# Performance work log

Measured on AMD Instinct MI355X. Metric: run time of the kernel, lower is better.

The kernel has to match this reference:

```python
import jax, jax.numpy as jnp
import numpy as np

BS, N, D, H = 4, 128, 768, 8
HD = D // H
FFN = 3072
E = BS * N * N
NORM_FACTOR = 100.0
NORM_CONST = 1.0
EPS_LN = 1e-5


def _ln(v, s, b):
    m = jnp.mean(v, -1, keepdims=True)
    var = jnp.mean(jnp.square(v - m), -1, keepdims=True)
    return (v - m) * jax.lax.rsqrt(var + EPS_LN) * s + b


def _glu(v, w, b):
    a, g = jnp.split(v @ w.T + b, 2, axis=-1)
    return a * jnp.square(jax.nn.relu(g))  # GLU with ReLU^2 gate activation


def setup_inputs() -> dict:
    key = jax.random.key(0)
    ks = jax.random.split(key, 24)
    rn = lambda i, shape, s=1.0: jax.random.normal(ks[i], shape, jnp.float32) * s
    # fully-connected per-graph edge_index with block structure
    base = jnp.arange(BS, dtype=jnp.int32) * N
    ii = jnp.repeat(jnp.arange(N, dtype=jnp.int32), N)
    jj = jnp.tile(jnp.arange(N, dtype=jnp.int32), N)
    row = (base[:, None] + ii[None, :]).reshape(-1)
    col = (base[:, None] + jj[None, :]).reshape(-1)
    edge_index = jnp.stack([row, col], 0)  # [2, E]
    return {
        'h': rn(0, (BS * N, D)),
        'x': rn(1, (BS * N, 3)),
        'edge_attr': rn(2, (E, 1)),
        'node_mask': jnp.ones((BS * N, 1), jnp.float32),
        'edge_mask': jnp.ones((E, 1), jnp.float32),
        'linker_mask': jnp.ones((BS * N, 1), jnp.float32),
        'in_proj_w': rn(3, (3 * D, D), 0.02), 'in_proj_b': jnp.zeros((3 * D,)),
        'out_proj_w': rn(4, (D, D), 0.02), 'out_proj_b': jnp.zeros((D,)),
        'ln1_s': jnp.ones((D,)), 'ln1_b': jnp.zeros((D,)),
        'ln2_s': jnp.ones((D,)), 'ln2_b': jnp.zeros((D,)),
        'fc1_w': rn(5, (2 * FFN, D), 0.02), 'fc1_b': jnp.zeros((2 * FFN,)),
        'fc2_w': rn(6, (2 * D, FFN), 0.02), 'fc2_b': jnp.zeros((2 * D,)),
        'efc1_w': rn(7, (H, 2), 0.5), 'efc1_b': jnp.zeros((H,)),
        'efc2_w': rn(8, (H, 2), 0.5), 'efc2_b': jnp.zeros((H,)),
        'cm1_w': rn(9, (D, 2 * D + 2), 0.02), 'cm1_b': jnp.zeros((D,)),
        'cm2_w': rn(10, (D, D), 0.02), 'cm2_b': jnp.zeros((D,)),
        'cm3_w': rn(11, (1, D), 0.001),
        'edge_index': edge_index,
    }


def _forward(h, x, edge_attr, node_mask, edge_mask, linker_mask,
             in_proj_w, in_proj_b, out_proj_w, out_proj_b,
             ln1_s, ln1_b, ln2_s, ln2_b, fc1_w, fc1_b, fc2_w, fc2_b,
             efc1_w, efc1_b, efc2_w, efc2_b,
             cm1_w, cm1_b, cm2_w, cm2_b, cm3_w, edge_index):
    row, col = edge_index[0], edge_index[1]
    # coord2diff
    diff = x[row] - x[col]                                   # [E,3]
    radial = jnp.sum(jnp.square(diff), 1, keepdims=True)     # [E,1]
    coord_diff = diff / (jnp.sqrt(radial + 1e-8) + NORM_CONST)
    ea = jnp.concatenate([radial, edge_attr], 1)             # [E,2]

    def edge_to_heads(w, b):
        y = (ea @ w.T + b) * edge_mask                       # [E,H]
        return jnp.transpose(y.reshape(BS, N, N, H), (0, 3, 1, 2))  # [BS,H,N,N]

    attn_bias = edge_to_heads(efc1_w, efc1_b)
    gw = edge_to_heads(efc2_w, efc2_b)

    # Graphormer3DEncoderLayer (eval mode: dropout = identity)
    hb = h.reshape(BS, N, D)
    hn = _ln(hb, ln1_s, ln1_b)
    q, k, v = jnp.split(hn @ in_proj_w.T + in_proj_b, 3, axis=-1)
    q = q.reshape(BS, N, H, HD) * (HD ** -0.5)
    k = k.reshape(BS, N, H, HD)
    v = v.reshape(BS, N, H, HD)
    scores = jnp.einsum('bihd,bjhd->bhij', q, k) + attn_bias
    probs = jnp.tanh(gw) * jax.nn.softmax(scores, axis=-1)   # tanh-gated softmax
    att = jnp.einsum('bhij,bjhd->bihd', probs, v).reshape(BS, N, D)
    h1 = hb + (att @ out_proj_w.T + out_proj_b)
    ff = _ln(h1, ln2_s, ln2_b)
    ff = jax.nn.gelu(_glu(ff, fc1_w, fc1_b), approximate=False)
    ff = _glu(ff, fc2_w, fc2_b)
    h_out = (h1 + ff).reshape(BS * N, D) * node_mask

    # EquivariantUpdate (tanh=False branch)
    ei = jnp.concatenate([h_out[row], h_out[col], ea], 1)    # [E, 2D+2]
    t = jax.nn.silu(ei @ cm1_w.T + cm1_b)
    t = jax.nn.silu(t @ cm2_w.T + cm2_b)
    s = t @ cm3_w.T                                          # [E,1]
    trans = coord_diff * s * edge_mask
    agg = jax.ops.segment_sum(trans, row, num_segments=BS * N) / NORM_FACTOR
    x_out = (x + agg * linker_mask) * node_mask
    return h_out, x_out


def reference(h, x, edge_attr, node_mask, edge_mask, linker_mask,
              in_proj_w, in_proj_b, out_proj_w, out_proj_b,
              ln1_s, ln1_b, ln2_s, ln2_b, fc1_w, fc1_b, fc2_w, fc2_b,
              efc1_w, efc1_b, efc2_w, efc2_b,
              cm1_w, cm1_b, cm2_w, cm2_b, cm3_w, edge_index):
    return _forward(h, x, edge_attr, node_mask, edge_mask, linker_mask,
                    in_proj_w, in_proj_b, out_proj_w, out_proj_b,
                    ln1_s, ln1_b, ln2_s, ln2_b, fc1_w, fc1_b, fc2_w, fc2_b,
                    efc1_w, efc1_b, efc2_w, efc2_b,
                    cm1_w, cm1_b, cm2_w, cm2_b, cm3_w, edge_index)
```

## Files before the change

kernel.cpp:

```cpp
#include <hip/hip_runtime.h>
#include <cstdint>
#include <cstddef>

#define BSZ   4
#define NN    128
#define DD    768
#define HH    8
#define HD    96
#define FFN   3072
#define NNODE (BSZ*NN)
#define NE    (NNODE*NN)

typedef unsigned short u16;
typedef __bf16 bf16x8 __attribute__((ext_vector_type(8)));
typedef float  f32x4  __attribute__((ext_vector_type(4)));
typedef unsigned short u16x8 __attribute__((ext_vector_type(8)));
typedef unsigned short u16x4 __attribute__((ext_vector_type(4)));
typedef unsigned short u16x2 __attribute__((ext_vector_type(2)));

__device__ __forceinline__ float bf2f(u16 a){
    unsigned u = ((unsigned)a) << 16; float f; __builtin_memcpy(&f, &u, 4); return f;
}
__device__ __forceinline__ u16 f2bf(float f){
    unsigned u; __builtin_memcpy(&u, &f, 4);
// ... 200 lines not shown

template<int MODE>
__global__ __launch_bounds__(256) void gemm_glu2(const u16* __restrict__ A, int lda,
                                                 const u16* __restrict__ B, int ldb,
                                                 const float* __restrict__ bias, int half_off, int K,
                                                 const float* __restrict__ h1f,
                                                 const float* __restrict__ nodemask,
                                                 u16* __restrict__ Cb, int ldc,
                                                 float* __restrict__ Cf){
    __shared__ u16 As[2][64 * 64];
    __shared__ u16 Ba[2][64 * 64];
    __shared__ u16 Bg[2][64 * 64];
    GEMM_PRO(A + (size_t)m0 * lda, B + (size_t)n0 * ldb)
    const u16* Gbase = B + (size_t)(half_off + n0) * ldb;
    f32x4 accA[2][2], accG[2][2];
    #pragma unroll
    for (int i = 0; i < 2; i++)
        #pragma unroll
        for (int j = 0; j < 2; j++){ f32x4 z = {0.f,0.f,0.f,0.f}; accA[i][j] = z; accG[i][j] = z; }

    stage64(As[0], Abase, lda, 0, tid);
    stage64(Ba[0], Bbase, ldb, 0, tid);
    stage64(Bg[0], Gbase, ldb, 0, tid);
    __syncthreads();
    const int NS = K / 64;
    #pragma unroll 1
    for (int s = 0; s < NS; s++){
        const int cur = s & 1;
        if (s + 1 < NS){
            stage64(As[cur ^ 1], Abase, lda, (s + 1) * 64, tid);
            stage64(Ba[cur ^ 1], Bbase, ldb, (s + 1) * 64, tid);
            stage64(Bg[cur ^ 1], Gbase, ldb, (s + 1) * 64, tid);
        }
        const char* ab = (const char*)&As[cur][0];
        const char* bab = (const char*)&Ba[cur][0];
        const char* bgb = (const char*)&Bg[cur][0];
        #pragma unroll
        for (int k0 = 0; k0 < 64; k0 += 32){
            const int kbx = ((k0 + quad * 8) * 2) ^ swz;
            bf16x8 a0  = frag((const u16*)(ab + (wy * 32 + l15) * 128 + kbx));
            bf16x8 a1  = frag((const u16*)(ab + (wy * 32 + 16 + l15) * 128 + kbx));
            bf16x8 ba0 = frag((const u16*)(bab + (wx * 32 + l15) * 128 + kbx));
            bf16x8 ba1 = frag((const u16*)(bab + (wx * 32 + 16 + l15) * 128 + kbx));
            bf16x8 bg0 = frag((const u16*)(bgb + (wx * 32 + l15) * 128 + kbx));
            bf16x8 bg1 = frag((const u16*)(bgb + (wx * 32 + 16 + l15) * 128 + kbx));
            accA[0][0] = mfma16(a0, ba0, accA[0][0]);
            accA[0][1] = mfma16(a0, ba1, accA[0][1]);
            accA[1][0] = mfma16(a1, ba0, accA[1][0]);
            accA[1][1] = mfma16(a1, ba1, accA[1][1]);
            accG[0][0] = mfma16(a0, bg0, accG[0][0]);
            accG[0][1] = mfma16(a0, bg1, accG[0][1]);
            accG[1][0] = mfma16(a1, bg0, accG[1][0]);
            accG[1][1] = mfma16(a1, bg1, accG[1][1]);
        }
        __syncthreads();
    }
    #pragma unroll
    for (int j = 0; j < 2; j++){
        int n = n0 + wx * 32 + j * 16 + l15;
        float bva = bias[n];
        float bvg = bias[half_off + n];
        #pragma unroll
        for (int i = 0; i < 2; i++){
            #pragma unroll
            for (int r = 0; r < 4; r++){
                int m = m0 + wy * 32 + i * 16 + quad * 4 + r;
                float a = accA[i][j][r] + bva;
                float g = accG[i][j][r] + bvg;
                float rg = fmaxf(g, 0.f);
                float t = a * rg * rg;
                if (MODE == 0){
                    float v = 0.5f * t * (1.f + erff(t * 0.70710678118654752f));
                    Cb[(size_t)m * ldc + n] = f2bf(v);
                } else {
                    float v = (t + h1f[(size_t)m * DD + n]) * nodemask[m];
                    Cf[(size_t)m * DD + n] = v;
                    Cb[(size_t)m * DD + n] = f2bf(v);
                }
            }
        }
    }
}

__global__ __launch_bounds__(256) void gemm_bt(const u16* __restrict__ A, int lda,
                                               const float* __restrict__ B, int ldb,
                                               const float* __restrict__ bias,
                                               u16* __restrict__ C, int ldc, int K){
    __shared__ u16 As[64 * 72];
    __shared__ u16 Bs[64 * 72];
    const int tid = threadIdx.x;
    const int m0 = blockIdx.y * 64, n0 = blockIdx.x * 64;
    const int w = tid >> 6, lane = tid & 63, quad = lane >> 4, l15 = lane & 15;
    const int wy = w >> 1, wx = w & 1;
    f32x4 acc[2][2];
    #pragma unroll
    for (int i = 0; i < 2; i++)
        #pragma unroll
        for (int j = 0; j < 2; j++){ f32x4 z = {0.f,0.f,0.f,0.f}; acc[i][j] = z; }

    for (int kk = 0; kk < K; kk += 64){
        stageA(As, A, m0, lda, kk, tid);
        stageBf32(Bs, B, n0, ldb, kk, tid);
        __syncthreads();
        #pragma unroll
        for (int k0 = 0; k0 < 64; k0 += 32){
            int kb = k0 + quad * 8;
            bf16x8 a0 = frag(&As[(wy * 32 + l15) * 72 + kb]);
            bf16x8 a1 = frag(&As[(wy * 32 + 16 + l15) * 72 + kb]);
            bf16x8 b0 = frag(&Bs[(wx * 32 + l15) * 72 + kb]);
            bf16x8 b1 = frag(&Bs[(wx * 32 + 16 + l15) * 72 + kb]);
            acc[0][0] = mfma16(a0, b0, acc[0][0]);
            acc[0][1] = mfma16(a0, b1, acc[0][1]);
            acc[1][0] = mfma16(a1, b0, acc[1][0]);
            acc[1][1] = mfma16(a1, b1, acc[1][1]);
        }
        __syncthreads();
    }
    #pragma unroll
    for (int j = 0; j < 2; j++){
        int n = n0 + wx * 32 + j * 16 + l15;
        float bv = bias[n];
        #pragma unroll
        for (int i = 0; i < 2; i++){
            #pragma unroll
            for (int r = 0; r < 4; r++){
                int m = m0 + wy * 32 + i * 16 + quad * 4 + r;
                C[(size_t)m * ldc + n] = f2bf(acc[i][j][r] + bv);
            }
        }
    }
}

__global__ __launch_bounds__(256) void gemm_proj(const u16* __restrict__ A,
                                                 const float* __restrict__ B,
                                                 const float* __restrict__ bias,
                                                 const float* __restrict__ h,
                                                 float* __restrict__ h1f){
    __shared__ u16 As[64 * 72];
    __shared__ u16 Bs[64 * 72];
    const int tid = threadIdx.x;
    const int m0 = blockIdx.y * 64, n0 = blockIdx.x * 64;
    const int w = tid >> 6, lane = tid & 63, quad = lane >> 4, l15 = lane & 15;
    const int wy = w >> 1, wx = w & 1;
    f32x4 acc[2][2];
    #pragma unroll
    for (int i = 0; i < 2; i++)
        #pragma unroll
        for (int j = 0; j < 2; j++){ f32x4 z = {0.f,0.f,0.f,0.f}; acc[i][j] = z; }

    for (int kk = 0; kk < DD; kk += 64){
        stageA(As, A, m0, DD, kk, tid);
        stageBf32(Bs, B, n0, DD, kk, tid);
        __syncthreads();
        #pragma unroll
        for (int k0 = 0; k0 < 64; k0 += 32){
            int kb = k0 + quad * 8;
            bf16x8 a0 = frag(&As[(wy * 32 + l15) * 72 + kb]);
            bf16x8 a1 = frag(&As[(wy * 32 + 16 + l15) * 72 + kb]);
            bf16x8 b0 = frag(&Bs[(wx * 32 + l15) * 72 + kb]);
            bf16x8 b1 = frag(&Bs[(wx * 32 + 16 + l15) * 72 + kb]);
            acc[0][0] = mfma16(a0, b0, acc[0][0]);
            acc[0][1] = mfma16(a0, b1, acc[0][1]);
            acc[1][0] = mfma16(a1, b0, acc[1][0]);
            acc[1][1] = mfma16(a1, b1, acc[1][1]);
        }
        __syncthreads();
// ... 74 lines not shown
                float rg = fmaxf(g, 0.f);
                float t = a * rg * rg;
                if (MODE == 0){
                    float v = 0.5f * t * (1.f + erff(t * 0.70710678118654752f));
                    Cb[(size_t)m * ldc + n] = f2bf(v);
                } else {
                    float v = (t + h1f[(size_t)m * DD + n]) * nodemask[m];
                    Cf[(size_t)m * DD + n] = v;
                    Cb[(size_t)m * DD + n] = f2bf(v);
                }
            }
        }
    }
}

__global__ __launch_bounds__(256) void gemm_pq(const u16* __restrict__ A,
                                               const float* __restrict__ W,
                                               const float* __restrict__ bias,
                                               u16* __restrict__ C){
    __shared__ u16 As[64 * 72];
    __shared__ u16 Bp[64 * 72];
    __shared__ u16 Bq[64 * 72];
    const int tid = threadIdx.x;
    const int m0 = blockIdx.y * 64, n0 = blockIdx.x * 64;
    const int w = tid >> 6, lane = tid & 63, quad = lane >> 4, l15 = lane & 15;
    const int wy = w >> 1, wx = w & 1;
    f32x4 accP[2][2], accQ[2][2];
    #pragma unroll
    for (int i = 0; i < 2; i++)
        #pragma unroll
        for (int j = 0; j < 2; j++){ f32x4 z = {0.f,0.f,0.f,0.f}; accP[i][j] = z; accQ[i][j] = z; }

    for (int kk = 0; kk < DD; kk += 64){
        stageA(As, A, m0, DD, kk, tid);
        #pragma unroll
        for (int p = 0; p < 8; p++){
            int idx = p * 256 + tid;
            int row = idx >> 5, c2 = idx & 31;
            size_t base = (size_t)(n0 + row) * 1538 + kk + c2 * 2;
            float2 vp = *(const float2*)(W + base);
            float2 vq = *(const float2*)(W + base + 768);
            u16x2 op; op[0] = f2bf(vp.x); op[1] = f2bf(vp.y);
            u16x2 oq; oq[0] = f2bf(vq.x); oq[1] = f2bf(vq.y);
            *(u16x2*)&Bp[row * 72 + c2 * 2] = op;
            *(u16x2*)&Bq[row * 72 + c2 * 2] = oq;
        }
        __syncthreads();
        #pragma unroll
        for (int k0 = 0; k0 < 64; k0 += 32){
            int kb = k0 + quad * 8;
            bf16x8 a0  = frag(&As[(wy * 32 + l15) * 72 + kb]);
            bf16x8 a1  = frag(&As[(wy * 32 + 16 + l15) * 72 + kb]);
            bf16x8 bp0 = frag(&Bp[(wx * 32 + l15) * 72 + kb]);
            bf16x8 bp1 = frag(&Bp[(wx * 32 + 16 + l15) * 72 + kb]);
            bf16x8 bq0 = frag(&Bq[(wx * 32 + l15) * 72 + kb]);
            bf16x8 bq1 = frag(&Bq[(wx * 32 + 16 + l15) * 72 + kb]);
            accP[0][0] = mfma16(a0, bp0, accP[0][0]);
            accP[0][1] = mfma16(a0, bp1, accP[0][1]);
            accP[1][0] = mfma16(a1, bp0, accP[1][0]);
            accP[1][1] = mfma16(a1, bp1, accP[1][1]);
            accQ[0][0] = mfma16(a0, bq0, accQ[0][0]);
            accQ[0][1] = mfma16(a0, bq1, accQ[0][1]);
            accQ[1][0] = mfma16(a1, bq0, accQ[1][0]);
            accQ[1][1] = mfma16(a1, bq1, accQ[1][1]);
        }
        __syncthreads();
    }
    #pragma unroll
    for (int j = 0; j < 2; j++){
        int n = n0 + wx * 32 + j * 16 + l15;
        float bv = bias[n];
        #pragma unroll
        for (int i = 0; i < 2; i++){
            #pragma unroll
            for (int r = 0; r < 4; r++){
                int m = m0 + wy * 32 + i * 16 + quad * 4 + r;
                C[(size_t)m * 1536 + n]       = f2bf(accP[i][j][r] + bv);
                C[(size_t)m * 1536 + 768 + n] = f2bf(accQ[i][j][r]);
            }
        }
    }
}

__global__ __launch_bounds__(128) void attn_k(const u16* __restrict__ qkv,
                                              const float* __restrict__ x,
                                              const float* __restrict__ eattr,
                                              const float* __restrict__ emask,
                                              const float* __restrict__ e1w, const float* __restrict__ e1b,
                                              const float* __restrict__ e2w, const float* __restrict__ e2b,
                                              u16* __restrict__ att){
    __shared__ u16 Ks[NN * 98];
    __shared__ u16 Vs[NN * 98];
    __shared__ float xs[NN * 3];
    __shared__ float qs[HD];
    __shared__ float ps[NN];
    __shared__ float red[2];
    const int tid = threadIdx.x;
    const int h = blockIdx.y, b = blockIdx.z;
    const int i0 = blockIdx.x * 16;

    for (int idx = tid; idx < NN * HD; idx += 128){
        int j = idx / HD, d = idx - j * HD;
        const u16* base = qkv + (size_t)(b * NN + j) * 2304 + h * HD + d;
        Ks[j * 98 + d] = base[DD];
        Vs[j * 98 + d] = base[1536];
    }
    if (tid < NN){
        xs[tid * 3]     = x[(b * NN + tid) * 3];
        xs[tid * 3 + 1] = x[(b * NN + tid) * 3 + 1];
        xs[tid * 3 + 2] = x[(b * NN + tid) * 3 + 2];
    }
    __syncthreads();
    const float w1r = e1w[h * 2], w1a = e1w[h * 2 + 1], b1 = e1b[h];
    const float w2r = e2w[h * 2], w2a = e2w[h * 2 + 1], b2v = e2b[h];
    const int wv = tid >> 6;

    for (int ig = 0; ig < 16; ig++){
        const int i = i0 + ig, ni = b * NN + i;
        if (tid < HD) qs[tid] = bf2f(qkv[(size_t)ni * 2304 + h * HD + tid]) * 0.10206207261596577f;
        __syncthreads();
        const int j = tid;
        float s = 0.f;
        #pragma unroll 8
        for (int d = 0; d < HD; d++) s += qs[d] * bf2f(Ks[j * 98 + d]);
        float d0 = xs[i * 3]     - xs[j * 3];
        float d1 = xs[i * 3 + 1] - xs[j * 3 + 1];
        float d2 = xs[i * 3 + 2] - xs[j * 3 + 2];
        float radial = d0*d0 + d1*d1 + d2*d2;
        int e = ni * NN + j;
        float at = eattr[e], em = emask[e];
        s += (w1r * radial + w1a * at + b1) * em;
        float gw = (w2r * radial + w2a * at + b2v) * em;
        float m1 = wred_max(s);
        if ((tid & 63) == 0) red[wv] = m1;
        __syncthreads();
        float M = fmaxf(red[0], red[1]);
        __syncthreads();
        float ev = __expf(s - M);
        float s1 = wred_sum(ev);
        if ((tid & 63) == 0) red[wv] = s1;
        __syncthreads();
        float S = red[0] + red[1];
        ps[j] = tanhf(gw) * ev / S;
        __syncthreads();
        if (tid < HD){
            float a = 0.f;
            #pragma unroll 8
            for (int jj = 0; jj < NN; jj++) a += ps[jj] * bf2f(Vs[jj * 98 + tid]);
            att[(size_t)ni * DD + h * HD + tid] = f2bf(a);
        }
        __syncthreads();
    }
}

__global__ void prep_k(const float* __restrict__ cm1w, float* __restrict__ c01){
    int idx = blockIdx.x * 256 + threadIdx.x;
    if (idx < 768){
        c01[idx]       = cm1w[(size_t)idx * 1538 + 1536];
        c01[768 + idx] = cm1w[(size_t)idx * 1538 + 1537];
    }
}

__global__ void w2bf_k(const float* __restrict__ W, u16* __restrict__ O, int n){
    int i4 = (blockIdx.x * 256 + threadIdx.x) * 4;
    if (i4 < n){
        float4 v = *(const float4*)(W + i4);
        u16x4 o; o[0] = f2bf(v.x); o[1] = f2bf(v.y); o[2] = f2bf(v.z); o[3] = f2bf(v.w);
        *(u16x4*)&O[i4] = o;
    }
}

__global__ __launch_bounds__(256) void t1_k(const u16* __restrict__ PQ,
                                            const float* __restrict__ c01,
                                            const float* __restrict__ x,
                                            const float* __restrict__ eattr,
                                            u16* __restrict__ T1g){
    int cid = blockIdx.x * 256 + threadIdx.x;
    int e = cid / 96;
    int kc = cid - e * 96;
    int k = kc * 8;
    int r = e >> 7;
    int j = e & 127;
    int b = r >> 7;
    int nc = b * NN + j;
    float d0 = x[r * 3]     - x[nc * 3];
    float d1 = x[r * 3 + 1] - x[nc * 3 + 1];
    float d2 = x[r * 3 + 2] - x[nc * 3 + 2];
    float rad = d0 * d0 + d1 * d1 + d2 * d2;
    float at = eattr[e];
    u16x8 pv = *(const u16x8*)(PQ + (size_t)r  * 1536 + k);
    u16x8 qv = *(const u16x8*)(PQ + (size_t)nc * 1536 + 768 + k);
    float4 c0a = *(const float4*)(c01 + k);
    float4 c0b = *(const float4*)(c01 + k + 4);
    float4 c1a = *(const float4*)(c01 + 768 + k);
    float4 c1b = *(const float4*)(c01 + 768 + k + 4);
    float c0r[8] = {c0a.x,c0a.y,c0a.z,c0a.w,c0b.x,c0b.y,c0b.z,c0b.w};
    float c1r[8] = {c1a.x,c1a.y,c1a.z,c1a.w,c1b.x,c1b.y,c1b.z,c1b.w};
    u16x8 ov;
    #pragma unroll
    for (int t = 0; t < 8; t++){
        float f = bf2f(pv[t]) + bf2f(qv[t]) + rad * c0r[t] + at * c1r[t];
        ov[t] = f2bf(fsilu(f));
    }
    *(u16x8*)&T1g[(size_t)e * 768 + k] = ov;
}

__global__ __launch_bounds__(512) void edge_k(const u16* __restrict__ T1g,
                                              const u16* __restrict__ W2b,
                                              const float* __restrict__ b2,
                                              const float* __restrict__ w3,
                                              const float* __restrict__ x,
                                              const float* __restrict__ emask,
                                              float* __restrict__ aggpart){
    __shared__ u16 Bd[2][384 * 64];
    __shared__ u16 T1d[2][128 * 64];
    __shared__ float sacc[128];
    __shared__ float red6[6];
    const int tid = threadIdx.x;
    const int r = blockIdx.x;
    const int b = r >> 7;

    if (tid < 128) sacc[tid] = 0.f;

    auto stageB = [&](int np, int kk, int p){
        #pragma unroll
        for (int c = 0; c < 6; c++){
            int idx = c * 512 + tid;
            int row = idx >> 3, ch = idx & 7;
            int sch = ch ^ (row & 7);
            gload16(W2b + (size_t)(np * 384 + row) * 768 + kk + sch * 8, &Bd[p][idx * 8]);
        }
    };
    auto stageT1 = [&](int kk, int p){
        #pragma unroll
        for (int c = 0; c < 2; c++){
            int idx = c * 512 + tid;
            int row = idx >> 3, ch = idx & 7;
            int sch = ch ^ (row & 7);
            gload16(T1g + (size_t)(r * NN + row) * 768 + kk + sch * 8, &T1d[p][idx * 8]);
        }
    };

    const int w = tid >> 6, lane = tid & 63, quad = lane >> 4, l15 = lane & 15;
    const int wr = w >> 2, wc = w & 3;
    const int swz = (l15 & 7) << 4;
    f32x4 acc[4][6];

    stageB(0, 0, 0);
    stageT1(0, 0);
    __syncthreads();

    #pragma unroll 1
    for (int np = 0; np < 2; np++){
        #pragma unroll
        for (int i = 0; i < 4; i++)
            #pragma unroll
            for (int jj = 0; jj < 6; jj++){ f32x4 z = {0.f,0.f,0.f,0.f}; acc[i][jj] = z; }

        #pragma unroll 1
        for (int kk64 = 0; kk64 < 12; kk64++){
            const int cur = kk64 & 1;
            const int s  = np * 12 + kk64;
            const int ns = s + 1;
            const int nkk = (kk64 == 11) ? 0 : kk64 + 1;
            const int nnp = (kk64 == 11) ? np + 1 : np;
            if (ns < 24){
                stageB(nnp, nkk * 64, nkk & 1);
                stageT1(nkk * 64, nkk & 1);
            }
            const char* tb = (const char*)&T1d[cur][0];
            const char* bb = (const char*)&Bd[cur][0];
            #pragma unroll
            for (int k0 = 0; k0 < 64; k0 += 32){
                const int kbx = ((k0 + quad * 8) * 2) ^ swz;
                bf16x8 aF[4], bF[6];
                #pragma unroll
                for (int i = 0; i < 4; i++)
                    aF[i] = frag((const u16*)(tb + (wr * 64 + i * 16 + l15) * 128 + kbx));
                #pragma unroll
                for (int jj = 0; jj < 6; jj++)
                    bF[jj] = frag((const u16*)(bb + (wc * 96 + jj * 16 + l15) * 128 + kbx));
                #pragma unroll
                for (int i = 0; i < 4; i++)
                    #pragma unroll
                    for (int jj = 0; jj < 6; jj++)
                        acc[i][jj] = mfma16(aF[i], bF[jj], acc[i][jj]);
            }
            __syncthreads();
        }

        float part[4][4];
        #pragma unroll
        for (int i = 0; i < 4; i++)
            #pragma unroll
            for (int rr = 0; rr < 4; rr++) part[i][rr] = 0.f;
        #pragma unroll
        for (int jj = 0; jj < 6; jj++){
            int n = np * 384 + wc * 96 + jj * 16 + l15;
            float bb2 = b2[n], cc = w3[n];
            #pragma unroll
            for (int i = 0; i < 4; i++)
                #pragma unroll
                for (int rr = 0; rr < 4; rr++){
                    float v = fsilu(acc[i][jj][rr] + bb2);
                    part[i][rr] += v * cc;
                }
        }
        #pragma unroll
        for (int i = 0; i < 4; i++)
            #pragma unroll
            for (int rr = 0; rr < 4; rr++){
                float v = part[i][rr];
                v += __shfl_xor(v, 1); v += __shfl_xor(v, 2);
                v += __shfl_xor(v, 4); v += __shfl_xor(v, 8);
                if (l15 == 0) atomicAdd(&sacc[wr * 64 + i * 16 + quad * 4 + rr], v);
            }
    }
    __syncthreads();
    if (tid < 128){
        const float xr0 = x[r * 3], xr1 = x[r * 3 + 1], xr2 = x[r * 3 + 2];
        int nc = b * NN + tid;
        float d0 = xr0 - x[nc * 3], d1 = xr1 - x[nc * 3 + 1], d2 = xr2 - x[nc * 3 + 2];
        float radial = d0 * d0 + d1 * d1 + d2 * d2;
        float inv = 1.f / (sqrtf(radial + 1e-8f) + 1.f);
        float sv = sacc[tid] * emask[r * NN + tid];
        float tx = d0 * inv * sv, ty = d1 * inv * sv, tz = d2 * inv * sv;
        #pragma unroll
        for (int m = 1; m < 64; m <<= 1){
            tx += __shfl_xor(tx, m); ty += __shfl_xor(ty, m); tz += __shfl_xor(tz, m);
        }
        if (lane == 0){
            red6[w * 3 + 0] = tx; red6[w * 3 + 1] = ty; red6[w * 3 + 2] = tz;
        }
    }
    __syncthreads();
    if (tid == 0){
        aggpart[r * 3 + 0] = red6[0] + red6[3];
        aggpart[r * 3 + 1] = red6[1] + red6[4];
        aggpart[r * 3 + 2] = red6[2] + red6[5];
    }
}

__global__ __launch_bounds__(512) void edge_fb_k(const u16* __restrict__ PQ,
                                                 const u16* __restrict__ W2b,
                                                 const float* __restrict__ b2,
                                                 const float* __restrict__ w3,
                                                 const float* __restrict__ c01,
                                                 const float* __restrict__ x,
                                                 const float* __restrict__ eattr,
                                                 const float* __restrict__ emask,
                                                 float* __restrict__ aggpart){
    __shared__ u16 Bd[2][192 * 64];
    __shared__ u16 T1s[128 * 64];
    __shared__ float sacc[128];
    __shared__ float red6[6];
    const int tid = threadIdx.x;
    const int r = blockIdx.x;
    const int b = r >> 7;

    const float xr0 = x[r * 3], xr1 = x[r * 3 + 1], xr2 = x[r * 3 + 2];
    const int jl0 = tid >> 3, jl1 = 64 + jl0;
    float rad0, eat0, rad1, eat1;
    {
        int nc0 = b * NN + jl0;
        float d0 = xr0 - x[nc0 * 3], d1 = xr1 - x[nc0 * 3 + 1], d2 = xr2 - x[nc0 * 3 + 2];
        rad0 = d0 * d0 + d1 * d1 + d2 * d2;
        eat0 = eattr[r * NN + jl0];
        int nc1 = b * NN + jl1;
        float e0 = xr0 - x[nc1 * 3], e1 = xr1 - x[nc1 * 3 + 1], e2 = xr2 - x[nc1 * 3 + 2];
        rad1 = e0 * e0 + e1 * e1 + e2 * e2;
        eat1 = eattr[r * NN + jl1];
    }
    if (tid < 128) sacc[tid] = 0.f;

    auto stageB = [&](int np, int kk, int p){
        #pragma unroll
        for (int c = 0; c < 3; c++){
            int idx = c * 512 + tid;
            int row = idx >> 3, ch = idx & 7;
            int sch = ch ^ (row & 7);
            gload16(W2b + (size_t)(np * 192 + row) * 768 + kk + sch * 8, &Bd[p][idx * 8]);
        }
    };
    auto stageT1 = [&](int kk){
        const int kc = tid & 7, k = kc * 8;
        float4 c0a = *(const float4*)(c01 + kk + k);
        float4 c0b = *(const float4*)(c01 + kk + k + 4);
        float4 c1a = *(const float4*)(c01 + 768 + kk + k);
        float4 c1b = *(const float4*)(c01 + 768 + kk + k + 4);
        float c0r[8] = {c0a.x,c0a.y,c0a.z,c0a.w,c0b.x,c0b.y,c0b.z,c0b.w};
        float c1r[8] = {c1a.x,c1a.y,c1a.z,c1a.w,c1b.x,c1b.y,c1b.z,c1b.w};
        u16x8 pv = *(const u16x8*)(PQ + (size_t)r * 1536 + kk + k);
        #pragma unroll
        for (int c = 0; c < 2; c++){
            int jl = c ? jl1 : jl0;
            float rj = c ? rad1 : rad0;
            float aj = c ? eat1 : eat0;
            int nc = b * NN + jl;
            u16x8 qv = *(const u16x8*)(PQ + (size_t)nc * 1536 + 768 + kk + k);
            u16x8 ov;
            #pragma unroll
            for (int t = 0; t < 8; t++){
// ... 67 lines not shown
        #pragma unroll
        for (int i = 0; i < 2; i++)
            #pragma unroll
            for (int rr = 0; rr < 4; rr++){
                float v = part[i][rr];
                v += __shfl_xor(v, 1); v += __shfl_xor(v, 2);
                v += __shfl_xor(v, 4); v += __shfl_xor(v, 8);
                if (l15 == 0) atomicAdd(&sacc[wr * 32 + i * 16 + quad * 4 + rr], v);
            }
    }
    __syncthreads();
    if (tid < 128){
        int nc = b * NN + tid;
        float d0 = xr0 - x[nc * 3], d1 = xr1 - x[nc * 3 + 1], d2 = xr2 - x[nc * 3 + 2];
        float radial = d0 * d0 + d1 * d1 + d2 * d2;
        float inv = 1.f / (sqrtf(radial + 1e-8f) + 1.f);
        float sv = sacc[tid] * emask[r * NN + tid];
        float tx = d0 * inv * sv, ty = d1 * inv * sv, tz = d2 * inv * sv;
        #pragma unroll
        for (int m = 1; m < 64; m <<= 1){
            tx += __shfl_xor(tx, m); ty += __shfl_xor(ty, m); tz += __shfl_xor(tz, m);
        }
        if (lane == 0){
            red6[w * 3 + 0] = tx; red6[w * 3 + 1] = ty; red6[w * 3 + 2] = tz;
        }
    }
    __syncthreads();
    if (tid == 0){
        aggpart[r * 3 + 0] = red6[0] + red6[3];
        aggpart[r * 3 + 1] = red6[1] + red6[4];
        aggpart[r * 3 + 2] = red6[2] + red6[5];
    }
}

__global__ void xout_k(const float* __restrict__ x, const float* __restrict__ linker,
                       const float* __restrict__ nodemask, const float* __restrict__ aggpart,
                       float* __restrict__ out){
    int idx = blockIdx.x * 256 + threadIdx.x;
    if (idx >= NNODE * 3) return;
    int node = idx / 3, c = idx - node * 3;
    float s = aggpart[node * 3 + c];
    out[(size_t)NNODE * DD + idx] = (x[idx] + s * 0.01f * linker[node]) * nodemask[node];
}

extern "C" void kernel_launch(void* const* d_in, const int* in_sizes, int n_in,
                              void* d_out, int out_size, void* d_ws, size_t ws_size,
                              hipStream_t stream){
    (void)in_sizes; (void)n_in; (void)out_size;
    const float* h        = (const float*)d_in[0];
    const float* x        = (const float*)d_in[1];
    const float* eattr    = (const float*)d_in[2];
    const float* nodemask = (const float*)d_in[3];
    const float* emask    = (const float*)d_in[4];
    const float* linker   = (const float*)d_in[5];
    const float* in_w  = (const float*)d_in[6];  const float* in_b  = (const float*)d_in[7];
    const float* out_w = (const float*)d_in[8];  const float* out_b = (const float*)d_in[9];
    const float* ln1s  = (const float*)d_in[10]; const float* ln1b  = (const float*)d_in[11];
    const float* ln2s  = (const float*)d_in[12]; const float* ln2b  = (const float*)d_in[13];
    const float* fc1w  = (const float*)d_in[14]; const float* fc1b  = (const float*)d_in[15];
    const float* fc2w  = (const float*)d_in[16]; const float* fc2b  = (const float*)d_in[17];
    const float* e1w   = (const float*)d_in[18]; const float* e1b   = (const float*)d_in[19];
    const float* e2w   = (const float*)d_in[20]; const float* e2b   = (const float*)d_in[21];
    const float* cm1w  = (const float*)d_in[22]; const float* cm1b  = (const float*)d_in[23];
    const float* cm2w  = (const float*)d_in[24]; const float* cm2b  = (const float*)d_in[25];
    const float* cm3w  = (const float*)d_in[26];
    float* out = (float*)d_out;

    char* ws = (char*)d_ws;
    u16*   hn      = (u16*)  (ws + 0);
    u16*   qkv     = (u16*)  (ws + 786432);
    u16*   att     = (u16*)  (ws + 3145728);
    float* h1f     = (float*)(ws + 0);
    u16*   ffin    = (u16*)  (ws + 1572864);
    u16*   g1      = (u16*)  (ws + 2359296);
    u16*   houtb   = (u16*)  (ws + 5505024);
    u16*   PQ      = (u16*)  (ws + 0);
    float* c01     = (float*)(ws + 1572864);
    float* aggpart = (float*)(ws + 1579008);
    u16*   cm2b16  = (u16*)  (ws + 6291456);
    u16*   in_wb   = (u16*)  (ws + 8388608);
    u16*   out_wb  = (u16*)  (ws + 11927552);
    u16*   fc1b16  = (u16*)  (ws + 13107200);
    u16*   fc2b16  = (u16*)  (ws + 22544384);
    u16*   T1g     = (u16*)  (ws + 8388608);
    const bool fast = ws_size >= (size_t)8388608 + (size_t)100663296;

    if (fast){
        w2bf_k <<<1728, 256, 0, stream>>>(in_w,  in_wb,  2304*768);
        w2bf_k <<<576,  256, 0, stream>>>(out_w, out_wb, 768*768);
        w2bf_k <<<4608, 256, 0, stream>>>(fc1w,  fc1b16, 6144*768);
        w2bf_k <<<4608, 256, 0, stream>>>(fc2w,  fc2b16, 1536*3072);
    }
    ln_k       <<<NNODE, 256, 0, stream>>>(h, ln1s, ln1b, hn);
    if (fast){
        gemm_bt2    <<<dim3(2304/64, NNODE/64), 256, 0, stream>>>(hn, DD, in_wb, DD, in_b, qkv, 2304, DD);
        attn_k      <<<dim3(NN/16, HH, BSZ), 128, 0, stream>>>(qkv, x, eattr, emask, e1w, e1b, e2w, e2b, att);
        gemm_proj2  <<<dim3(DD/64, NNODE/64), 256, 0, stream>>>(att, out_wb, out_b, h, h1f);
        ln_k        <<<NNODE, 256, 0, stream>>>(h1f, ln2s, ln2b, ffin);
        gemm_glu2<0><<<dim3(FFN/64, NNODE/64), 256, 0, stream>>>(ffin, DD, fc1b16, DD, fc1b, FFN, DD,
                                                                 nullptr, nullptr, g1, FFN, nullptr);
        gemm_glu2<1><<<dim3(DD/64, NNODE/64), 256, 0, stream>>>(g1, FFN, fc2b16, FFN, fc2b, DD, FFN,
                                                                h1f, nodemask, houtb, DD, out);
    } else {
        gemm_bt    <<<dim3(2304/64, NNODE/64), 256, 0, stream>>>(hn, DD, in_w, DD, in_b, qkv, 2304, DD);
        attn_k     <<<dim3(NN/16, HH, BSZ), 128, 0, stream>>>(qkv, x, eattr, emask, e1w, e1b, e2w, e2b, att);
        gemm_proj  <<<dim3(DD/64, NNODE/64), 256, 0, stream>>>(att, out_w, out_b, h, h1f);
        ln_k       <<<NNODE, 256, 0, stream>>>(h1f, ln2s, ln2b, ffin);
        gemm_glu<0><<<dim3(FFN/64, NNODE/64), 256, 0, stream>>>(ffin, DD, fc1w, DD, fc1b, FFN, DD,
                                                                nullptr, nullptr, g1, FFN, nullptr);
        gemm_glu<1><<<dim3(DD/64, NNODE/64), 256, 0, stream>>>(g1, FFN, fc2w, FFN, fc2b, DD, FFN,
                                                               h1f, nodemask, houtb, DD, out);
    }
    prep_k     <<<3, 256, 0, stream>>>(cm1w, c01);
    w2bf_k     <<<576, 256, 0, stream>>>(cm2w, cm2b16, DD*DD);
    gemm_pq    <<<dim3(DD/64, NNODE/64), 256, 0, stream>>>(houtb, cm1w, cm1b, PQ);
    if (fast){
        t1_k   <<<24576, 256, 0, stream>>>(PQ, c01, x, eattr, T1g);
        edge_k <<<512, 512, 0, stream>>>(T1g, cm2b16, cm2b, cm3w, x, emask, aggpart);
    } else {
        edge_fb_k<<<512, 512, 0, stream>>>(PQ, cm2b16, cm2b, cm3w, c01, x, eattr, emask, aggpart);
    }
    xout_k     <<<6, 256, 0, stream>>>(x, linker, nodemask, aggpart, out);
}
```

Before: 451.0 us.

## Triple-buffer edge GEMM, vectorize attention K/V loads, fuse weight conversions

The edge MLP kernel moves from double to triple buffering with 256-column N tiles over three passes. It uses explicit vmcnt waits and raw s_barrier so loads for two stages ahead overlap with MFMA work. The attention kernel now loads and reads K/V rows with 16-byte vectors and a padded stride of 104. The five fp32-to-bf16 weight conversion launches are merged into one kernel to cut launch overhead. In exchange, the edge kernel holds fewer accumulators per pass and runs an extra pass, and the manual waitcnt logic depends on exact load counts.

```diff
diff --git a/kernel.cpp b/kernel.cpp
--- a/kernel.cpp
+++ b/kernel.cpp
@@ -546,6 +546,7 @@
     }
 }
 
+#define KSTR 104
 __global__ __launch_bounds__(128) void attn_k(const u16* __restrict__ qkv,
                                               const float* __restrict__ x,
                                               const float* __restrict__ eattr,
@@ -553,8 +554,8 @@
                                               const float* __restrict__ e1w, const float* __restrict__ e1b,
                                               const float* __restrict__ e2w, const float* __restrict__ e2b,
                                               u16* __restrict__ att){
-    __shared__ u16 Ks[NN * 98];
-    __shared__ u16 Vs[NN * 98];
+    __shared__ u16 Ks[NN * KSTR];
+    __shared__ u16 Vs[NN * KSTR];
     __shared__ float xs[NN * 3];
     __shared__ float qs[HD];
     __shared__ float ps[NN];
@@ -563,11 +564,11 @@
     const int h = blockIdx.y, b = blockIdx.z;
     const int i0 = blockIdx.x * 16;
 
-    for (int idx = tid; idx < NN * HD; idx += 128){
-        int j = idx / HD, d = idx - j * HD;
-        const u16* base = qkv + (size_t)(b * NN + j) * 2304 + h * HD + d;
-        Ks[j * 98 + d] = base[DD];
-        Vs[j * 98 + d] = base[1536];
+    for (int idx = tid; idx < NN * 12; idx += 128){
+        int j = idx / 12, c = idx - j * 12;
+        const u16* base = qkv + (size_t)(b * NN + j) * 2304 + h * HD + c * 8;
+        *(u16x8*)&Ks[j * KSTR + c * 8] = *(const u16x8*)(base + DD);
+        *(u16x8*)&Vs[j * KSTR + c * 8] = *(const u16x8*)(base + 1536);
     }
     if (tid < NN){
         xs[tid * 3]     = x[(b * NN + tid) * 3];
@@ -585,8 +586,12 @@
         __syncthreads();
         const int j = tid;
         float s = 0.f;
-        #pragma unroll 8
-        for (int d = 0; d < HD; d++) s += qs[d] * bf2f(Ks[j * 98 + d]);
+        #pragma unroll
+        for (int c = 0; c < 12; c++){
+            u16x8 kv = *(const u16x8*)&Ks[j * KSTR + c * 8];
+            #pragma unroll
+            for (int t = 0; t < 8; t++) s += qs[c * 8 + t] * bf2f(kv[t]);
+        }
         float d0 = xs[i * 3]     - xs[j * 3];
         float d1 = xs[i * 3 + 1] - xs[j * 3 + 1];
         float d2 = xs[i * 3 + 2] - xs[j * 3 + 2];
@@ -610,7 +615,7 @@
         if (tid < HD){
             float a = 0.f;
             #pragma unroll 8
-            for (int jj = 0; jj < NN; jj++) a += ps[jj] * bf2f(Vs[jj * 98 + tid]);
+            for (int jj = 0; jj < NN; jj++) a += ps[jj] * bf2f(Vs[jj * KSTR + tid]);
             att[(size_t)ni * DD + h * HD + tid] = f2bf(a);
         }
         __syncthreads();
@@ -632,6 +637,27 @@
         u16x4 o; o[0] = f2bf(v.x); o[1] = f2bf(v.y); o[2] = f2bf(v.z); o[3] = f2bf(v.w);
         *(u16x4*)&O[i4] = o;
     }
+}
+
+__global__ void w2bf5_k(const float* __restrict__ a0, u16* __restrict__ o0, int s0,
+                        const float* __restrict__ a1, u16* __restrict__ o1, int s1,
+                        const float* __restrict__ a2, u16* __restrict__ o2, int s2,
+                        const float* __restrict__ a3, u16* __restrict__ o3, int s3,
+                        const float* __restrict__ a4, u16* __restrict__ o4, int s4){
+    int off = (blockIdx.x * 256 + threadIdx.x) * 4;
+    const float* s; u16* d;
+    if (off < s0){ s = a0; d = o0; }
+    else { off -= s0;
+    if (off < s1){ s = a1; d = o1; }
+    else { off -= s1;
+    if (off < s2){ s = a2; d = o2; }
+    else { off -= s2;
+    if (off < s3){ s = a3; d = o3; }
+    else { off -= s3;
+    if (off >= s4) return; s = a4; d = o4; }}}}
+    float4 v = *(const float4*)(s + off);
+    u16x4 o; o[0] = f2bf(v.x); o[1] = f2bf(v.y); o[2] = f2bf(v.z); o[3] = f2bf(v.w);
+    *(u16x4*)&d[off] = o;
 }
 
 __global__ __launch_bounds__(256) void t1_k(const u16* __restrict__ PQ,
@@ -676,81 +702,81 @@
                                               const float* __restrict__ x,
                                               const float* __restrict__ emask,
                                               float* __restrict__ aggpart){
-    __shared__ u16 Bd[2][384 * 64];
-    __shared__ u16 T1d[2][128 * 64];
+    __shared__ u16 Bd[3][256 * 64];
+    __shared__ u16 T1d[3][128 * 64];
     __shared__ float sacc[128];
     __shared__ float red6[6];
     const int tid = threadIdx.x;
     const int r = blockIdx.x;
-    const int b = r >> 7;
 
     if (tid < 128) sacc[tid] = 0.f;
 
-    auto stageB = [&](int np, int kk, int p){
-        #pragma unroll
-        for (int c = 0; c < 6; c++){
+    auto stage = [&](int s){
+        int snp = s / 12;
+        int skk = (s - snp * 12) * 64;
+        int p = s % 3;
+        #pragma unroll
+        for (int c = 0; c < 4; c++){
             int idx = c * 512 + tid;
             int row = idx >> 3, ch = idx & 7;
             int sch = ch ^ (row & 7);
-            gload16(W2b + (size_t)(np * 384 + row) * 768 + kk + sch * 8, &Bd[p][idx * 8]);
-        }
-    };
-    auto stageT1 = [&](int kk, int p){
+            gload16(W2b + (size_t)(snp * 256 + row) * 768 + skk + sch * 8, &Bd[p][idx * 8]);
+        }
         #pragma unroll
         for (int c = 0; c < 2; c++){
             int idx = c * 512 + tid;
             int row = idx >> 3, ch = idx & 7;
             int sch = ch ^ (row & 7);
-            gload16(T1g + (size_t)(r * NN + row) * 768 + kk + sch * 8, &T1d[p][idx * 8]);
+            gload16(T1g + (size_t)(r * NN + row) * 768 + skk + sch * 8, &T1d[p][idx * 8]);
         }
     };
 
     const int w = tid >> 6, lane = tid & 63, quad = lane >> 4, l15 = lane & 15;
     const int wr = w >> 2, wc = w & 3;
     const int swz = (l15 & 7) << 4;
-    f32x4 acc[4][6];
-
-    stageB(0, 0, 0);
-    stageT1(0, 0);
-    __syncthreads();
+    f32x4 acc[4][4];
+
+    stage(0);
+    stage(1);
+    __builtin_amdgcn_sched_barrier(0);
+    asm volatile("s_waitcnt vmcnt(6)" ::: "memory");
+    __builtin_amdgcn_s_barrier();
+    __builtin_amdgcn_sched_barrier(0);
 
     #pragma unroll 1
-    for (int np = 0; np < 2; np++){
+    for (int np = 0; np < 3; np++){
         #pragma unroll
         for (int i = 0; i < 4; i++)
             #pragma unroll
-            for (int jj = 0; jj < 6; jj++){ f32x4 z = {0.f,0.f,0.f,0.f}; acc[i][jj] = z; }
+            for (int jj = 0; jj < 4; jj++){ f32x4 z = {0.f,0.f,0.f,0.f}; acc[i][jj] = z; }
 
         #pragma unroll 1
         for (int kk64 = 0; kk64 < 12; kk64++){
-            const int cur = kk64 & 1;
-            const int s  = np * 12 + kk64;
-            const int ns = s + 1;
-            const int nkk = (kk64 == 11) ? 0 : kk64 + 1;
-            const int nnp = (kk64 == 11) ? np + 1 : np;
-            if (ns < 24){
-                stageB(nnp, nkk * 64, nkk & 1);
-                stageT1(nkk * 64, nkk & 1);
-            }
-            const char* tb = (const char*)&T1d[cur][0];
-            const char* bb = (const char*)&Bd[cur][0];
+            const int s = np * 12 + kk64;
+            if (s + 2 < 36) stage(s + 2);
+            const char* tb = (const char*)&T1d[s % 3][0];
+            const char* bb = (const char*)&Bd[s % 3][0];
             #pragma unroll
             for (int k0 = 0; k0 < 64; k0 += 32){
                 const int kbx = ((k0 + quad * 8) * 2) ^ swz;
-                bf16x8 aF[4], bF[6];
+                bf16x8 aF[4], bF[4];
                 #pragma unroll
                 for (int i = 0; i < 4; i++)
                     aF[i] = frag((const u16*)(tb + (wr * 64 + i * 16 + l15) * 128 + kbx));
                 #pragma unroll
-                for (int jj = 0; jj < 6; jj++)
-                    bF[jj] = frag((const u16*)(bb + (wc * 96 + jj * 16 + l15) * 128 + kbx));
+                for (int jj = 0; jj < 4; jj++)
+                    bF[jj] = frag((const u16*)(bb + (wc * 64 + jj * 16 + l15) * 128 + kbx));
                 #pragma unroll
                 for (int i = 0; i < 4; i++)
                     #pragma unroll
-                    for (int jj = 0; jj < 6; jj++)
+                    for (int jj = 0; jj < 4; jj++)
                         acc[i][jj] = mfma16(aF[i], bF[jj], acc[i][jj]);
             }
-            __syncthreads();
+            __builtin_amdgcn_sched_barrier(0);
+            if (s + 2 < 36){ asm volatile("s_waitcnt vmcnt(6)" ::: "memory"); }
+            else           { asm volatile("s_waitcnt vmcnt(0)" ::: "memory"); }
+            __builtin_amdgcn_s_barrier();
+            __builtin_amdgcn_sched_barrier(0);
         }
 
         float part[4][4];
@@ -759,8 +785,8 @@
             #pragma unroll
             for (int rr = 0; rr < 4; rr++) part[i][rr] = 0.f;
         #pragma unroll
-        for (int jj = 0; jj < 6; jj++){
-            int n = np * 384 + wc * 96 + jj * 16 + l15;
+        for (int jj = 0; jj < 4; jj++){
+            int n = np * 256 + wc * 64 + jj * 16 + l15;
             float bb2 = b2[n], cc = w3[n];
             #pragma unroll
             for (int i = 0; i < 4; i++)
@@ -782,6 +808,7 @@
     }
     __syncthreads();
     if (tid < 128){
+        const int b = r >> 7;
         const float xr0 = x[r * 3], xr1 = x[r * 3 + 1], xr2 = x[r * 3 + 2];
         int nc = b * NN + tid;
         float d0 = xr0 - x[nc * 3], d1 = xr1 - x[nc * 3 + 1], d2 = xr2 - x[nc * 3 + 2];
@@ -1019,10 +1046,13 @@
     const bool fast = ws_size >= (size_t)8388608 + (size_t)100663296;
 
     if (fast){
-        w2bf_k <<<1728, 256, 0, stream>>>(in_w,  in_wb,  2304*768);
-        w2bf_k <<<576,  256, 0, stream>>>(out_w, out_wb, 768*768);
-        w2bf_k <<<4608, 256, 0, stream>>>(fc1w,  fc1b16, 6144*768);
-        w2bf_k <<<4608, 256, 0, stream>>>(fc2w,  fc2b16, 1536*3072);
+        w2bf5_k <<<12096, 256, 0, stream>>>(in_w,  in_wb,  2304*768,
+                                            out_w, out_wb, 768*768,
+                                            fc1w,  fc1b16, 6144*768,
+                                            fc2w,  fc2b16, 1536*3072,
+                                            cm2w,  cm2b16, 768*768);
+    } else {
+        w2bf_k <<<576, 256, 0, stream>>>(cm2w, cm2b16, DD*DD);
     }
     ln_k       <<<NNODE, 256, 0, stream>>>(h, ln1s, ln1b, hn);
     if (fast){
@@ -1045,7 +1075,6 @@
                                                                h1f, nodemask, houtb, DD, out);
     }
     prep_k     <<<3, 256, 0, stream>>>(cm1w, c01);
-    w2bf_k     <<<576, 256, 0, stream>>>(cm2w, cm2b16, DD*DD);
     gemm_pq    <<<dim3(DD/64, NNODE/64), 256, 0, stream>>>(houtb, cm1w, cm1b, PQ);
     if (fast){
         t1_k   <<<24576, 256, 0, stream>>>(PQ, c01, x, eattr, T1g);
```

New measurement: 461.7 us. 2.4% more time.

## Batch weight conversions, add bf16 double-buffered PQ GEMM, vectorize attention K/V loads

Applied to the files above, without the earlier changes.

Merges the five fp32-to-bf16 weight conversion launches into one kernel, which cuts launch overhead. The cm1 P/Q halves are now pre-converted to bf16 so a new double-buffered MFMA GEMM (gemm_pq2) can replace the fp32-input gemm_pq. The attention kernel now stages K/V with 16-byte vector loads into padded shared rows of 104 elements and reads K vectorized in the dot product. The wpq buffer reuses the fc2b16 region after fc2 has finished, so correctness depends on that stream ordering.

```diff
diff --git a/kernel.cpp b/kernel.cpp
--- a/kernel.cpp
+++ b/kernel.cpp
@@ -306,6 +306,84 @@
     }
 }
 
+__global__ __launch_bounds__(256) void gemm_pq2(const u16* __restrict__ A,
+                                                const u16* __restrict__ Wpq,
+                                                const float* __restrict__ bias,
+                                                u16* __restrict__ C){
+    __shared__ u16 As[2][64 * 64];
+    __shared__ u16 Bp[2][64 * 64];
+    __shared__ u16 Bq[2][64 * 64];
+    GEMM_PRO(A + (size_t)m0 * DD, Wpq + (size_t)n0 * DD)
+    const u16* Gbase = Wpq + (size_t)(768 + n0) * DD;
+    f32x4 accP[2][2], accQ[2][2];
+    #pragma unroll
+    for (int i = 0; i < 2; i++)
+        #pragma unroll
+        for (int j = 0; j < 2; j++){ f32x4 z = {0.f,0.f,0.f,0.f}; accP[i][j] = z; accQ[i][j] = z; }
+
+    stage64(As[0], Abase, DD, 0, tid);
+    stage64(Bp[0], Bbase, DD, 0, tid);
+    stage64(Bq[0], Gbase, DD, 0, tid);
+    __syncthreads();
+    #pragma unroll 1
+    for (int s = 0; s < 12; s++){
+        const int cur = s & 1;
+        if (s + 1 < 12){
+            stage64(As[cur ^ 1], Abase, DD, (s + 1) * 64, tid);
+            stage64(Bp[cur ^ 1], Bbase, DD, (s + 1) * 64, tid);
+            stage64(Bq[cur ^ 1], Gbase, DD, (s + 1) * 64, tid);
+        }
+        const char* ab  = (const char*)&As[cur][0];
+        const char* bpb = (const char*)&Bp[cur][0];
+        const char* bqb = (const char*)&Bq[cur][0];
+        #pragma unroll
+        for (int k0 = 0; k0 < 64; k0 += 32){
+            const int kbx = ((k0 + quad * 8) * 2) ^ swz;
+            bf16x8 a0  = frag((const u16*)(ab + (wy * 32 + l15) * 128 + kbx));
+            bf16x8 a1  = frag((const u16*)(ab + (wy * 32 + 16 + l15) * 128 + kbx));
+            bf16x8 bp0 = frag((const u16*)(bpb + (wx * 32 + l15) * 128 + kbx));
+            bf16x8 bp1 = frag((const u16*)(bpb + (wx * 32 + 16 + l15) * 128 + kbx));
+            bf16x8 bq0 = frag((const u16*)(bqb + (wx * 32 + l15) * 128 + kbx));
+            bf16x8 bq1 = frag((const u16*)(bqb + (wx * 32 + 16 + l15) * 128 + kbx));
+            accP[0][0] = mfma16(a0, bp0, accP[0][0]);
+            accP[0][1] = mfma16(a0, bp1, accP[0][1]);
+            accP[1][0] = mfma16(a1, bp0, accP[1][0]);
+            accP[1][1] = mfma16(a1, bp1, accP[1][1]);
+            accQ[0][0] = mfma16(a0, bq0, accQ[0][0]);
+            accQ[0][1] = mfma16(a0, bq1, accQ[0][1]);
+            accQ[1][0] = mfma16(a1, bq0, accQ[1][0]);
+            accQ[1][1] = mfma16(a1, bq1, accQ[1][1]);
+        }
+        __syncthreads();
+    }
+    #pragma unroll
+    for (int j = 0; j < 2; j++){
+        int n = n0 + wx * 32 + j * 16 + l15;
+        float bv = bias[n];
+        #pragma unroll
+        for (int i = 0; i < 2; i++){
+            #pragma unroll
+            for (int r = 0; r < 4; r++){
+                int m = m0 + wy * 32 + i * 16 + quad * 4 + r;
+                C[(size_t)m * 1536 + n]       = f2bf(accP[i][j][r] + bv);
+                C[(size_t)m * 1536 + 768 + n] = f2bf(accQ[i][j][r]);
+            }
+        }
+    }
+}
+
+__global__ void pq2bf_k(const float* __restrict__ W, u16* __restrict__ O){
+    int idx = blockIdx.x * 256 + threadIdx.x;
+    if (idx >= 768 * 384) return;
+    int n = idx / 384, kp = idx - n * 384, k = kp * 2;
+    float2 vp = *(const float2*)(W + (size_t)n * 1538 + k);
+    float2 vq = *(const float2*)(W + (size_t)n * 1538 + 768 + k);
+    u16x2 op; op[0] = f2bf(vp.x); op[1] = f2bf(vp.y);
+    u16x2 oq; oq[0] = f2bf(vq.x); oq[1] = f2bf(vq.y);
+    *(u16x2*)&O[(size_t)n * 768 + k]         = op;
+    *(u16x2*)&O[(size_t)(768 + n) * 768 + k] = oq;
+}
+
 __global__ __launch_bounds__(256) void gemm_bt(const u16* __restrict__ A, int lda,
                                                const float* __restrict__ B, int ldb,
                                                const float* __restrict__ bias,
@@ -546,6 +624,7 @@
     }
 }
 
+#define KSTR 104
 __global__ __launch_bounds__(128) void attn_k(const u16* __restrict__ qkv,
                                               const float* __restrict__ x,
                                               const float* __restrict__ eattr,
@@ -553,8 +632,8 @@
                                               const float* __restrict__ e1w, const float* __restrict__ e1b,
                                               const float* __restrict__ e2w, const float* __restrict__ e2b,
                                               u16* __restrict__ att){
-    __shared__ u16 Ks[NN * 98];
-    __shared__ u16 Vs[NN * 98];
+    __shared__ u16 Ks[NN * KSTR];
+    __shared__ u16 Vs[NN * KSTR];
     __shared__ float xs[NN * 3];
     __shared__ float qs[HD];
     __shared__ float ps[NN];
@@ -563,11 +642,11 @@
     const int h = blockIdx.y, b = blockIdx.z;
     const int i0 = blockIdx.x * 16;
 
-    for (int idx = tid; idx < NN * HD; idx += 128){
-        int j = idx / HD, d = idx - j * HD;
-        const u16* base = qkv + (size_t)(b * NN + j) * 2304 + h * HD + d;
-        Ks[j * 98 + d] = base[DD];
-        Vs[j * 98 + d] = base[1536];
+    for (int idx = tid; idx < NN * 12; idx += 128){
+        int j = idx / 12, c = idx - j * 12;
+        const u16* base = qkv + (size_t)(b * NN + j) * 2304 + h * HD + c * 8;
+        *(u16x8*)&Ks[j * KSTR + c * 8] = *(const u16x8*)(base + DD);
+        *(u16x8*)&Vs[j * KSTR + c * 8] = *(const u16x8*)(base + 1536);
     }
     if (tid < NN){
         xs[tid * 3]     = x[(b * NN + tid) * 3];
@@ -585,8 +664,12 @@
         __syncthreads();
         const int j = tid;
         float s = 0.f;
-        #pragma unroll 8
-        for (int d = 0; d < HD; d++) s += qs[d] * bf2f(Ks[j * 98 + d]);
+        #pragma unroll
+        for (int c = 0; c < 12; c++){
+            u16x8 kv = *(const u16x8*)&Ks[j * KSTR + c * 8];
+            #pragma unroll
+            for (int t = 0; t < 8; t++) s += qs[c * 8 + t] * bf2f(kv[t]);
+        }
         float d0 = xs[i * 3]     - xs[j * 3];
         float d1 = xs[i * 3 + 1] - xs[j * 3 + 1];
         float d2 = xs[i * 3 + 2] - xs[j * 3 + 2];
@@ -610,7 +693,7 @@
         if (tid < HD){
             float a = 0.f;
             #pragma unroll 8
-            for (int jj = 0; jj < NN; jj++) a += ps[jj] * bf2f(Vs[jj * 98 + tid]);
+            for (int jj = 0; jj < NN; jj++) a += ps[jj] * bf2f(Vs[jj * KSTR + tid]);
             att[(size_t)ni * DD + h * HD + tid] = f2bf(a);
         }
         __syncthreads();
@@ -632,6 +715,27 @@
         u16x4 o; o[0] = f2bf(v.x); o[1] = f2bf(v.y); o[2] = f2bf(v.z); o[3] = f2bf(v.w);
         *(u16x4*)&O[i4] = o;
     }
+}
+
+__global__ void w2bf5_k(const float* __restrict__ a0, u16* __restrict__ o0, int s0,
+                        const float* __restrict__ a1, u16* __restrict__ o1, int s1,
+                        const float* __restrict__ a2, u16* __restrict__ o2, int s2,
+                        const float* __restrict__ a3, u16* __restrict__ o3, int s3,
+                        const float* __restrict__ a4, u16* __restrict__ o4, int s4){
+    int off = (blockIdx.x * 256 + threadIdx.x) * 4;
+    const float* s; u16* d;
+    if (off < s0){ s = a0; d = o0; }
+    else { off -= s0;
+    if (off < s1){ s = a1; d = o1; }
+    else { off -= s1;
+    if (off < s2){ s = a2; d = o2; }
+    else { off -= s2;
+    if (off < s3){ s = a3; d = o3; }
+    else { off -= s3;
+    if (off >= s4) return; s = a4; d = o4; }}}}
+    float4 v = *(const float4*)(s + off);
+    u16x4 o; o[0] = f2bf(v.x); o[1] = f2bf(v.y); o[2] = f2bf(v.z); o[3] = f2bf(v.w);
+    *(u16x4*)&d[off] = o;
 }
 
 __global__ __launch_bounds__(256) void t1_k(const u16* __restrict__ PQ,
@@ -1015,14 +1119,18 @@
     u16*   out_wb  = (u16*)  (ws + 11927552);
     u16*   fc1b16  = (u16*)  (ws + 13107200);
     u16*   fc2b16  = (u16*)  (ws + 22544384);
+    u16*   wpq     = (u16*)  (ws + 22544384);
     u16*   T1g     = (u16*)  (ws + 8388608);
     const bool fast = ws_size >= (size_t)8388608 + (size_t)100663296;
 
     if (fast){
-        w2bf_k <<<1728, 256, 0, stream>>>(in_w,  in_wb,  2304*768);
-        w2bf_k <<<576,  256, 0, stream>>>(out_w, out_wb, 768*768);
-        w2bf_k <<<4608, 256, 0, stream>>>(fc1w,  fc1b16, 6144*768);
-        w2bf_k <<<4608, 256, 0, stream>>>(fc2w,  fc2b16, 1536*3072);
+        w2bf5_k <<<12096, 256, 0, stream>>>(in_w,  in_wb,  2304*768,
+                                            out_w, out_wb, 768*768,
+                                            fc1w,  fc1b16, 6144*768,
+                                            fc2w,  fc2b16, 1536*3072,
+                                            cm2w,  cm2b16, 768*768);
+    } else {
+        w2bf_k <<<576, 256, 0, stream>>>(cm2w, cm2b16, DD*DD);
     }
     ln_k       <<<NNODE, 256, 0, stream>>>(h, ln1s, ln1b, hn);
     if (fast){
@@ -1045,12 +1153,13 @@
                                                                h1f, nodemask, houtb, DD, out);
     }
     prep_k     <<<3, 256, 0, stream>>>(cm1w, c01);
-    w2bf_k     <<<576, 256, 0, stream>>>(cm2w, cm2b16, DD*DD);
-    gemm_pq    <<<dim3(DD/64, NNODE/64), 256, 0, stream>>>(houtb, cm1w, cm1b, PQ);
     if (fast){
-        t1_k   <<<24576, 256, 0, stream>>>(PQ, c01, x, eattr, T1g);
-        edge_k <<<512, 512, 0, stream>>>(T1g, cm2b16, cm2b, cm3w, x, emask, aggpart);
+        pq2bf_k  <<<1152, 256, 0, stream>>>(cm1w, wpq);
+        gemm_pq2 <<<dim3(DD/64, NNODE/64), 256, 0, stream>>>(houtb, wpq, cm1b, PQ);
+        t1_k     <<<24576, 256, 0, stream>>>(PQ, c01, x, eattr, T1g);
+        edge_k   <<<512, 512, 0, stream>>>(T1g, cm2b16, cm2b, cm3w, x, emask, aggpart);
     } else {
+        gemm_pq  <<<dim3(DD/64, NNODE/64), 256, 0, stream>>>(houtb, cm1w, cm1b, PQ);
         edge_fb_k<<<512, 512, 0, stream>>>(PQ, cm2b16, cm2b, cm3w, c01, x, eattr, emask, aggpart);
     }
     xout_k     <<<6, 256, 0, stream>>>(x, linker, nodemask, aggpart, out);
```

Result: faster. 427.2 us (-5.3%).
